# Kernel tuning notes

Measured on AMD Instinct MI355X. Metric: run time of the kernel, lower is better.

## Reference

```python
import jax, jax.numpy as jnp
import numpy as np

D, H, E, K = 1024, 1024, 8, 2  # model dim, expert hidden dim, n_experts, top_k


def setup_inputs() -> dict:
    key = jax.random.key(0)
    ks = jax.random.split(key, 5)
    s = lambda k, shape, scale: jax.random.normal(k, shape, dtype=jnp.float32) * scale
    return {
        "input_batch": s(ks[0], (2, 512, D), 1.0),
        "router_w": s(ks[1], (D, E), D ** -0.5),
        "w_in": s(ks[2], (E, D, H), D ** -0.5),
        "b_in": jnp.zeros((E, H), jnp.float32),
        "w_out": s(ks[3], (E, H, D), H ** -0.5),
        "b_out": jnp.zeros((E, D), jnp.float32),
    }


def _moe(x, router_w, w_in, b_in, w_out, b_out):
    B, S, Dm = x.shape
    T = B * S
    x2 = x.reshape(T, Dm)
    # router: per-token logit scores over experts
    logits = x2 @ router_w                                # [T, E]
    probs = jax.nn.softmax(logits, axis=-1)
    # sampler: top-k experts per token
    top_p, top_e = jax.lax.top_k(probs, K)                # [T, K]
    flat_e = top_e.reshape(-1)                            # [N] with N = T*K
    flat_p = top_p.reshape(-1)
    tok = jnp.repeat(jnp.arange(T), K)                    # owning token of each dispatch row
    # sort dispatched rows by expert id (expert_sorted_indices in the original)
    order = jnp.argsort(flat_e)
    se, sp, st = flat_e[order], flat_p[order], tok[order]
    xd = x2[st]                                           # [N, D] gathered dispatch
    N = xd.shape[0]
    # per-expert 2-layer MLP; loop over the small fixed expert set with masking
    h = jnp.zeros((N, H), x.dtype)
    for e in range(E):
        m = (se == e)[:, None]
        h = h + jnp.where(m, jax.nn.gelu(xd @ w_in[e] + b_in[e]), 0.0)
    y = jnp.zeros((N, Dm), x.dtype)
    for e in range(E):
        m = (se == e)[:, None]
        y = y + jnp.where(m, h @ w_out[e] + b_out[e], 0.0)
    # weighted scatter-combine (index_add in the original)
    y = y * sp[:, None]
    out = jnp.zeros((T, Dm), x.dtype).at[st].add(y)
    return out.reshape(B, S, Dm)


def reference(input_batch, router_w, w_in, b_in, w_out, b_out):
    return _moe(input_batch, router_w, w_in, b_in, w_out, b_out)
```

## Files before the change

### kernel.cpp

```cpp
#include <hip/hip_runtime.h>
#include <hip/hip_bf16.h>

#define DM 1024
#define HD 1024
#define NE 8
#define NT 1024
#define NR 2048
#define BM 64
#define BN 64
#define BKK 64
#define LDK 72
#define MT_MAX 40
#define PN_MAX (MT_MAX * BM)
#define NBLK (MT_MAX * (HD / BN))
#define NXCD 8

typedef __attribute__((ext_vector_type(8))) short short8;
typedef __attribute__((ext_vector_type(4))) float f32x4;

typedef const __attribute__((address_space(1))) void* gas_ptr;
typedef __attribute__((address_space(3))) void* las_ptr;

__device__ __forceinline__ void glds16(const void* g, void* l) {
    __builtin_amdgcn_global_load_lds((gas_ptr)g, (las_ptr)l, 16, 0, 0);
}

__device__ __forceinline__ float gelu_tanh(float x) {
    float x3 = x * x * x;
    return 0.5f * x * (1.0f + tanhf(0.7978845608028654f * (x + 0.044715f * x3)));
}

__global__ __launch_bounds__(256) void moe_front(const float* __restrict__ x,
                                                 const float* __restrict__ rw,
                                                 const float* __restrict__ w_in,
                                                 const float* __restrict__ w_out,
                                                 int* __restrict__ e_sel,
                                                 float* __restrict__ p_sel,
                                                 __hip_bfloat16* __restrict__ wt1,
                                                 __hip_bfloat16* __restrict__ wt2) {
    __shared__ float ts[64][65];
    int bid = blockIdx.x;
    if (bid < 4096) {
        int ty = bid >> 8;
        int bx = bid & 255;
        const float* src = (ty < 8 ? w_in : w_out) + (size_t)(ty & 7) * DM * HD;
        unsigned short* dst = (unsigned short*)(ty < 8 ? wt1 : wt2) + (size_t)(ty & 7) * DM * HD;
        int k0 = (bx >> 4) * 64, n0 = (bx & 15) * 64;
        int r = threadIdx.x >> 4;
        int c = (threadIdx.x & 15) * 4;
#pragma unroll
        for (int i = 0; i < 4; ++i) {
            int rr = r + 16 * i;
            float4 f = *(const float4*)(src + (size_t)(k0 + rr) * HD + n0 + c);
            ts[rr][c] = f.x; ts[rr][c + 1] = f.y; ts[rr][c + 2] = f.z; ts[rr][c + 3] = f.w;
        }
        __syncthreads();
#pragma unroll
        for (int i = 0; i < 4; ++i) {
            int rn = r + 16 * i;
            __hip_bfloat16 b0 = __float2bfloat16(ts[c][rn]);
            __hip_bfloat16 b1 = __float2bfloat16(ts[c + 1][rn]);
            __hip_bfloat16 b2 = __float2bfloat16(ts[c + 2][rn]);
            __hip_bfloat16 b3 = __float2bfloat16(ts[c + 3][rn]);
            ushort4 u;
            u.x = *(unsigned short*)&b0; u.y = *(unsigned short*)&b1;
            u.z = *(unsigned short*)&b2; u.w = *(unsigned short*)&b3;
            *(ushort4*)(dst + (size_t)(n0 + rn) * DM + k0 + c) = u;
        }
    } else {
        int w = threadIdx.x >> 6;
        int lane = threadIdx.x & 63;
        int t = (bid - 4096) * 4 + w;
        const float* xr = x + (size_t)t * DM;
        float acc[NE];
#pragma unroll
        for (int e = 0; e < NE; ++e) acc[e] = 0.0f;
        for (int d = lane; d < DM; d += 64) {
            float xv = xr[d];
            const float* rp = rw + (size_t)d * NE;
#pragma unroll
            for (int e = 0; e < NE; ++e) acc[e] += xv * rp[e];
        }
#pragma unroll
        for (int e = 0; e < NE; ++e) {
#pragma unroll
            for (int off = 32; off > 0; off >>= 1) acc[e] += __shfl_xor(acc[e], off);
        }
        if (lane == 0) {
            float m = acc[0];
#pragma unroll
            for (int e = 1; e < NE; ++e) m = fmaxf(m, acc[e]);
            float p[NE];
            float s = 0.0f;
#pragma unroll
            for (int e = 0; e < NE; ++e) { p[e] = __expf(acc[e] - m); s += p[e]; }
            float inv = 1.0f / s;
            int i0 = 0;
#pragma unroll
            for (int e = 1; e < NE; ++e) if (p[e] > p[i0]) i0 = e;
            int i1 = (i0 == 0) ? 1 : 0;
#pragma unroll
            for (int e = 0; e < NE; ++e) if (e != i1 && e != i0 && p[e] > p[i1]) i1 = e;
            e_sel[2 * t + 0] = i0;
            e_sel[2 * t + 1] = i1;
            p_sel[2 * t + 0] = p[i0] * inv;
            p_sel[2 * t + 1] = p[i1] * inv;
        }
    }
}

__global__ void moe_router(const float* __restrict__ x, const float* __restrict__ rw,
                           int* __restrict__ e_sel, float* __restrict__ p_sel) {
    int t = blockIdx.x;
    int lane = threadIdx.x;
    const float* xr = x + (size_t)t * DM;
    float acc[NE];
#pragma unroll
    for (int e = 0; e < NE; ++e) acc[e] = 0.0f;
    for (int d = lane; d < DM; d += 64) {
        float xv = xr[d];
        const float* r = rw + (size_t)d * NE;
#pragma unroll
        for (int e = 0; e < NE; ++e) acc[e] += xv * r[e];
    }
#pragma unroll
    for (int e = 0; e < NE; ++e) {
#pragma unroll
        for (int off = 32; off > 0; off >>= 1) acc[e] += __shfl_xor(acc[e], off);
    }
    if (lane == 0) {
        float m = acc[0];
#pragma unroll
        for (int e = 1; e < NE; ++e) m = fmaxf(m, acc[e]);
        float p[NE];
        float s = 0.0f;
#pragma unroll
        for (int e = 0; e < NE; ++e) { p[e] = __expf(acc[e] - m); s += p[e]; }
        float inv = 1.0f / s;
        int i0 = 0;
#pragma unroll
        for (int e = 1; e < NE; ++e) if (p[e] > p[i0]) i0 = e;
        int i1 = (i0 == 0) ? 1 : 0;
#pragma unroll
        for (int e = 0; e < NE; ++e) if (e != i1 && e != i0 && p[e] > p[i1]) i1 = e;
        e_sel[2 * t + 0] = i0;
        e_sel[2 * t + 1] = i1;
        p_sel[2 * t + 0] = p[i0] * inv;
        p_sel[2 * t + 1] = p[i1] * inv;
    }
}

__global__ void moe_route_pack(const int* __restrict__ e_sel, int* __restrict__ meta,
                               int* __restrict__ sorted_tok, int* __restrict__ pos_of_row) {
    __shared__ int scnt[NE];
    __shared__ int soff[NE];
    int tid = threadIdx.x;
    if (tid < NE) scnt[tid] = 0;
    __syncthreads();
    for (int i = tid; i < NR; i += 256) atomicAdd(&scnt[e_sel[i]], 1);
    __syncthreads();
    if (tid == 0) {
        int off = 0, tc = 0;
        for (int e = 0; e < NE; ++e) {
            soff[e] = off;
            meta[8 + e] = off;
            int nt = (scnt[e] + BM - 1) / BM;
            for (int t = 0; t < nt; ++t) meta[16 + tc++] = e;
            off += nt * BM;
            scnt[e] = 0;
        }
        for (; tc < MT_MAX; ++tc) meta[16 + tc] = -1;
    }
    __syncthreads();
    for (int i = tid; i < PN_MAX; i += 256) sorted_tok[i] = -1;
    __syncthreads();
    for (int i = tid; i < NR; i += 256) {
        int e = e_sel[i];
        int r = atomicAdd(&scnt[e], 1);
        int pos = soff[e] + r;
        sorted_tok[pos] = i >> 1;
        pos_of_row[i] = pos;
    }
}

__global__ __launch_bounds__(256) void moe_gather(const float* __restrict__ x,
                                                  const int* __restrict__ sorted_tok,
                                                  __hip_bfloat16* __restrict__ xg) {
    int pos = blockIdx.x;
    int t = sorted_tok[pos];
    int j = threadIdx.x * 4;
    ushort4 u;
    if (t >= 0) {
        float4 f = *(const float4*)(x + (size_t)t * DM + j);
        __hip_bfloat16 b0 = __float2bfloat16(f.x), b1 = __float2bfloat16(f.y);
        __hip_bfloat16 b2 = __float2bfloat16(f.z), b3 = __float2bfloat16(f.w);
        u.x = *(unsigned short*)&b0; u.y = *(unsigned short*)&b1;
        u.z = *(unsigned short*)&b2; u.w = *(unsigned short*)&b3;
    } else {
        u.x = u.y = u.z = u.w = 0;
    }
    *(ushort4*)((unsigned short*)xg + (size_t)pos * DM + j) = u;
}

template <int EPI>
__global__ __launch_bounds__(256, 3) void moe_gemm_async(const __hip_bfloat16* __restrict__ A,
                                                         const __hip_bfloat16* __restrict__ Bt,
                                                         const float* __restrict__ bias,
                                                         const int* __restrict__ meta,
                                                         __hip_bfloat16* __restrict__ Hout,
                                                         float* __restrict__ Yout) {
    int bid = blockIdx.x;
    int swz = (bid % NXCD) * (NBLK / NXCD) + bid / NXCD;
    int mt = swz >> 4;
    int nb = swz & 15;
    int e = meta[16 + mt];
    if (e < 0) return;

    __shared__ __align__(16) unsigned char smem[3 * 16384];

    int tid = threadIdx.x;
    int wid = tid >> 6, lane = tid & 63;
    int wm = wid >> 1, wn = wid & 1;

    const unsigned short* Ab = (const unsigned short*)A + (size_t)mt * BM * DM;
    const unsigned short* Bb = (const unsigned short*)Bt + (size_t)e * DM * HD + (size_t)nb * BN * DM;

    int srow = wid * 16 + (lane >> 3);
    int s_log = (lane & 7) ^ (lane >> 3);
    const unsigned short* agp0 = Ab + (size_t)srow * DM + s_log * 8;
    const unsigned short* agp1 = agp0 + 8 * DM;
    const unsigned short* bgp0 = Bb + (size_t)srow * DM + s_log * 8;
    const unsigned short* bgp1 = bgp0 + 8 * DM;

    auto ISSUE = [&](int b, int kt) {
        unsigned char* sa = &smem[b * 16384 + wid * 2048];
        unsigned char* sb = &smem[b * 16384 + 8192 + wid * 2048];
        glds16(agp0 + kt * BKK, sa);
        glds16(agp1 + kt * BKK, sa + 1024);
        glds16(bgp0 + kt * BKK, sb);
        glds16(bgp1 + kt * BKK, sb + 1024);
    };

    int r16 = lane & 15, g = lane >> 4, l7 = lane & 7;
    int aoff[2][2], boff[2][2];
#pragma unroll
    for (int kk = 0; kk < 2; ++kk)
#pragma unroll
        for (int f = 0; f < 2; ++f) {
            int sw = (((kk << 2) + g) ^ l7) << 4;
            aoff[kk][f] = (wm * 32 + r16 + 16 * f) * 128 + sw;
            boff[kk][f] = (wn * 32 + r16 + 16 * f) * 128 + sw;
        }

    f32x4 acc[2][2] = {};

    ISSUE(0, 0);
    ISSUE(1, 1);
    ISSUE(2, 2);

#pragma unroll
    for (int kt = 0; kt < 16; ++kt) {
        if (kt <= 13)      asm volatile("s_waitcnt vmcnt(8)" ::: "memory");
        else if (kt == 14) asm volatile("s_waitcnt vmcnt(4)" ::: "memory");
        else               asm volatile("s_waitcnt vmcnt(0)" ::: "memory");
        asm volatile("s_barrier" ::: "memory");
        const unsigned char* sa = &smem[(kt % 3) * 16384];
        const unsigned char* sb = sa + 8192;
#pragma unroll
        for (int kk = 0; kk < 2; ++kk) {
            short8 a0 = *(const short8*)(sa + aoff[kk][0]);
            short8 a1 = *(const short8*)(sa + aoff[kk][1]);
            short8 b0 = *(const short8*)(sb + boff[kk][0]);
            short8 b1 = *(const short8*)(sb + boff[kk][1]);
            acc[0][0] = __builtin_amdgcn_mfma_f32_16x16x32_bf16(a0, b0, acc[0][0], 0, 0, 0);
            acc[0][1] = __builtin_amdgcn_mfma_f32_16x16x32_bf16(a0, b1, acc[0][1], 0, 0, 0);
            acc[1][0] = __builtin_amdgcn_mfma_f32_16x16x32_bf16(a1, b0, acc[1][0], 0, 0, 0);
            acc[1][1] = __builtin_amdgcn_mfma_f32_16x16x32_bf16(a1, b1, acc[1][1], 0, 0, 0);
        }
        asm volatile("s_barrier" ::: "memory");
        if (kt + 3 < 16) ISSUE(kt % 3, kt + 3);
    }

    int row0 = mt * BM + wm * 32 + ((lane >> 4) << 2);
    int col0 = nb * BN + wn * 32 + (lane & 15);
    const float* be = bias + (size_t)e * HD;
#pragma unroll
    for (int fm = 0; fm < 2; ++fm) {
#pragma unroll
        for (int fn = 0; fn < 2; ++fn) {
            int c = col0 + fn * 16;
            float bv = be[c];
#pragma unroll
            for (int r = 0; r < 4; ++r) {
                int rr = row0 + fm * 16 + r;
                float v = acc[fm][fn][r] + bv;
                if (EPI == 0) {
                    Hout[(size_t)rr * HD + c] = __float2bfloat16(gelu_tanh(v));
                } else {
                    Yout[(size_t)rr * HD + c] = v;
                }
            }
        }
    }
}

__global__ __launch_bounds__(256) void moe_combine(const float* __restrict__ y,
                                                   const float* __restrict__ p_sel,
                                                   const int* __restrict__ pos_of_row,
                                                   float* __restrict__ out) {
    int t = blockIdx.x;
    int j = threadIdx.x * 4;
    int q0 = pos_of_row[2 * t], q1 = pos_of_row[2 * t + 1];
    float p0 = p_sel[2 * t], p1 = p_sel[2 * t + 1];
    float4 a = *(const float4*)(y + (size_t)q0 * DM + j);
    float4 b = *(const float4*)(y + (size_t)q1 * DM + j);
    float4 o;
    o.x = p0 * a.x + p1 * b.x;
    o.y = p0 * a.y + p1 * b.y;
    o.z = p0 * a.z + p1 * b.z;
    o.w = p0 * a.w + p1 * b.w;
    *(float4*)(out + (size_t)t * DM + j) = o;
}

template <int EPI>
__global__ __launch_bounds__(256) void moe_gemm(const __hip_bfloat16* __restrict__ A,
                                                const float* __restrict__ W,
                                                const float* __restrict__ bias,
                                                const int* __restrict__ meta,
                                                __hip_bfloat16* __restrict__ Hout,
                                                float* __restrict__ Yout) {
    int mt = blockIdx.y;
    int e = meta[16 + mt];
    if (e < 0) return;
    int nb = blockIdx.x;
    __shared__ __align__(16) __hip_bfloat16 As[2][BM][LDK];
    __shared__ __align__(16) __hip_bfloat16 Bs[2][BN][LDK];
    int tid = threadIdx.x;
    int wid = tid >> 6, lane = tid & 63;
    int wm = wid >> 1, wn = wid & 1;
    const __hip_bfloat16* Ab = A + (size_t)mt * BM * DM;
    const float* Wb = W + (size_t)e * DM * HD + (size_t)nb * BN;
    uint4 ra[2];
    float4 rb[4];
    auto GLOAD = [&](int kt) {
#pragma unroll
        for (int i = 0; i < 2; ++i) {
            int c = tid + 256 * i;
            int row = c >> 3, col8 = c & 7;
            ra[i] = *(const uint4*)((const unsigned short*)Ab + (size_t)row * DM + kt * BKK + col8 * 8);
        }
#pragma unroll
        for (int i = 0; i < 4; ++i) {
            int c = tid + 256 * i;
            int kr = c >> 4, c4 = c & 15;
            rb[i] = *(const float4*)(Wb + (size_t)(kt * BKK + kr) * HD + c4 * 4);
        }
    };
    auto STORE = [&](int b) {
#pragma unroll
        for (int i = 0; i < 2; ++i) {
            int c = tid + 256 * i;
            int row = c >> 3, col8 = c & 7;
            *(uint4*)&As[b][row][col8 * 8] = ra[i];
        }
#pragma unroll
        for (int i = 0; i < 4; ++i) {
            int c = tid + 256 * i;
            int kr = c >> 4, c4 = c & 15;
            Bs[b][c4 * 4 + 0][kr] = __float2bfloat16(rb[i].x);
            Bs[b][c4 * 4 + 1][kr] = __float2bfloat16(rb[i].y);
            Bs[b][c4 * 4 + 2][kr] = __float2bfloat16(rb[i].z);
            Bs[b][c4 * 4 + 3][kr] = __float2bfloat16(rb[i].w);
        }
    };
    f32x4 acc[2][2] = {};
    GLOAD(0);
    STORE(0);
    __syncthreads();
    int buf = 0;
    const int NK = DM / BKK;
    for (int kt = 0; kt < NK; ++kt) {
        if (kt + 1 < NK) GLOAD(kt + 1);
#pragma unroll
        for (int kk = 0; kk < 2; ++kk) {
            int kb = kk * 32 + (lane >> 4) * 8;
            short8 a0 = *(const short8*)&As[buf][wm * 32 + (lane & 15)][kb];
            short8 a1 = *(const short8*)&As[buf][wm * 32 + 16 + (lane & 15)][kb];
            short8 b0 = *(const short8*)&Bs[buf][wn * 32 + (lane & 15)][kb];
            short8 b1 = *(const short8*)&Bs[buf][wn * 32 + 16 + (lane & 15)][kb];
            acc[0][0] = __builtin_amdgcn_mfma_f32_16x16x32_bf16(a0, b0, acc[0][0], 0, 0, 0);
            acc[0][1] = __builtin_amdgcn_mfma_f32_16x16x32_bf16(a0, b1, acc[0][1], 0, 0, 0);
            acc[1][0] = __builtin_amdgcn_mfma_f32_16x16x32_bf16(a1, b0, acc[1][0], 0, 0, 0);
            acc[1][1] = __builtin_amdgcn_mfma_f32_16x16x32_bf16(a1, b1, acc[1][1], 0, 0, 0);
        }
        if (kt + 1 < NK) {
            STORE(buf ^ 1);
            __syncthreads();
            buf ^= 1;
        }
    }
    int row0 = mt * BM + wm * 32 + ((lane >> 4) << 2);
    int col0 = nb * BN + wn * 32 + (lane & 15);
    const float* be = bias + (size_t)e * HD;
#pragma unroll
    for (int fm = 0; fm < 2; ++fm) {
#pragma unroll
        for (int fn = 0; fn < 2; ++fn) {
            int c = col0 + fn * 16;
            float bv = be[c];
#pragma unroll
            for (int r = 0; r < 4; ++r) {
                int rr = row0 + fm * 16 + r;
                float v = acc[fm][fn][r] + bv;
                if (EPI == 0) {
                    Hout[(size_t)rr * HD + c] = __float2bfloat16(gelu_tanh(v));
                } else {
                    Yout[(size_t)rr * HD + c] = v;
                }
            }
        }
    }
}

extern "C" void kernel_launch(void* const* d_in, const int* in_sizes, int n_in,
                              void* d_out, int out_size, void* d_ws, size_t ws_size,
                              hipStream_t stream) {
    const float* x     = (const float*)d_in[0];
    const float* rw    = (const float*)d_in[1];
    const float* w_in  = (const float*)d_in[2];
    const float* b_in  = (const float*)d_in[3];
    const float* w_out = (const float*)d_in[4];
    const float* b_out = (const float*)d_in[5];
    float* out = (float*)d_out;

    char* ws = (char*)d_ws;
    int*   e_sel      = (int*)ws;
    float* p_sel      = (float*)(ws + 8 * 1024);
    int*   meta       = (int*)(ws + 16 * 1024);
    int*   sorted_tok = (int*)(ws + 17 * 1024);
    int*   pos_of_row = (int*)(ws + 27 * 1024);

    const size_t SZ_X  = (size_t)PN_MAX * DM * 2;
    const size_t SZ_Y  = (size_t)PN_MAX * DM * 4;
    const size_t SZ_WT = (size_t)NE * DM * HD * 2;

    __hip_bfloat16* xg  = (__hip_bfloat16*)(ws + 64 * 1024);
    __hip_bfloat16* h   = (__hip_bfloat16*)(ws + 64 * 1024 + SZ_X);
    __hip_bfloat16* wt1 = (__hip_bfloat16*)(ws + 64 * 1024 + 2 * SZ_X);
    float*          y   = (float*)wt1;
    __hip_bfloat16* wt2 = (__hip_bfloat16*)(ws + 64 * 1024 + 2 * SZ_X + SZ_WT);

    const size_t NEED_FULL = 64 * 1024 + 2 * SZ_X + 2 * SZ_WT;
    const size_t NEED_FB   = 64 * 1024 + 2 * SZ_X + SZ_Y;

    if (ws_size >= NEED_FULL) {
        moe_front<<<4096 + NT / 4, 256, 0, stream>>>(x, rw, w_in, w_out, e_sel, p_sel, wt1, wt2);
        moe_route_pack<<<1, 256, 0, stream>>>(e_sel, meta, sorted_tok, pos_of_row);
        moe_gather<<<PN_MAX, 256, 0, stream>>>(x, sorted_tok, xg);
        moe_gemm_async<0><<<NBLK, 256, 0, stream>>>(xg, wt1, b_in, meta, h, nullptr);
        moe_gemm_async<1><<<NBLK, 256, 0, stream>>>(h, wt2, b_out, meta, nullptr, y);
        moe_combine<<<NT, 256, 0, stream>>>(y, p_sel, pos_of_row, out);
    } else if (ws_size >= NEED_FB) {
        float* y2 = (float*)(ws + 64 * 1024 + 2 * SZ_X);
        moe_router<<<NT, 64, 0, stream>>>(x, rw, e_sel, p_sel);
        moe_route_pack<<<1, 256, 0, stream>>>(e_sel, meta, sorted_tok, pos_of_row);
        moe_gather<<<PN_MAX, 256, 0, stream>>>(x, sorted_tok, xg);
        dim3 grid(HD / BN, MT_MAX);
        moe_gemm<0><<<grid, 256, 0, stream>>>(xg, w_in, b_in, meta, h, nullptr);
        moe_gemm<1><<<grid, 256, 0, stream>>>(h, w_out, b_out, meta, nullptr, y2);
        moe_combine<<<NT, 256, 0, stream>>>(y2, p_sel, pos_of_row, out);
    }
}
```

Before: 65.62 us.

## Fuse token gather into first GEMM via indirect row loads from bf16 token copy

The bf16 conversion of the input tokens moves into the front kernel, which writes a compact token copy plus one zero padding row. The separate gather kernel launch is removed. The first expert GEMM now reads A rows indirectly through sorted_tok, and padding slots point at the zero row. This removes one kernel launch and a full write and read of the gathered activation buffer, at the cost of scattered row addresses in the GEMM's async loads.

```diff
diff --git a/kernel.cpp b/kernel.cpp
--- a/kernel.cpp
+++ b/kernel.cpp
@@ -37,7 +37,8 @@
                                                  int* __restrict__ e_sel,
                                                  float* __restrict__ p_sel,
                                                  __hip_bfloat16* __restrict__ wt1,
-                                                 __hip_bfloat16* __restrict__ wt2) {
+                                                 __hip_bfloat16* __restrict__ wt2,
+                                                 __hip_bfloat16* __restrict__ xc) {
     __shared__ float ts[64][65];
     int bid = blockIdx.x;
     if (bid < 4096) {
@@ -67,7 +68,7 @@
             u.z = *(unsigned short*)&b2; u.w = *(unsigned short*)&b3;
             *(ushort4*)(dst + (size_t)(n0 + rn) * DM + k0 + c) = u;
         }
-    } else {
+    } else if (bid < 4096 + NT / 4) {
         int w = threadIdx.x >> 6;
         int lane = threadIdx.x & 63;
         int t = (bid - 4096) * 4 + w;
@@ -106,6 +107,20 @@
             p_sel[2 * t + 0] = p[i0] * inv;
             p_sel[2 * t + 1] = p[i1] * inv;
         }
+    } else {
+        int t = bid - (4096 + NT / 4);
+        int j = threadIdx.x * 4;
+        ushort4 u;
+        if (t < NT) {
+            float4 f = *(const float4*)(x + (size_t)t * DM + j);
+            __hip_bfloat16 b0 = __float2bfloat16(f.x), b1 = __float2bfloat16(f.y);
+            __hip_bfloat16 b2 = __float2bfloat16(f.z), b3 = __float2bfloat16(f.w);
+            u.x = *(unsigned short*)&b0; u.y = *(unsigned short*)&b1;
+            u.z = *(unsigned short*)&b2; u.w = *(unsigned short*)&b3;
+        } else {
+            u.x = u.y = u.z = u.w = 0;
+        }
+        *(ushort4*)((unsigned short*)xc + (size_t)t * DM + j) = u;
     }
 }
 
@@ -172,7 +187,7 @@
         for (; tc < MT_MAX; ++tc) meta[16 + tc] = -1;
     }
     __syncthreads();
-    for (int i = tid; i < PN_MAX; i += 256) sorted_tok[i] = -1;
+    for (int i = tid; i < PN_MAX; i += 256) sorted_tok[i] = NT;
     __syncthreads();
     for (int i = tid; i < NR; i += 256) {
         int e = e_sel[i];
@@ -190,7 +205,7 @@
     int t = sorted_tok[pos];
     int j = threadIdx.x * 4;
     ushort4 u;
-    if (t >= 0) {
+    if (t >= 0 && t < NT) {
         float4 f = *(const float4*)(x + (size_t)t * DM + j);
         __hip_bfloat16 b0 = __float2bfloat16(f.x), b1 = __float2bfloat16(f.y);
         __hip_bfloat16 b2 = __float2bfloat16(f.z), b3 = __float2bfloat16(f.w);
@@ -202,11 +217,12 @@
     *(ushort4*)((unsigned short*)xg + (size_t)pos * DM + j) = u;
 }
 
-template <int EPI>
+template <int EPI, int INDIR>
 __global__ __launch_bounds__(256, 3) void moe_gemm_async(const __hip_bfloat16* __restrict__ A,
                                                          const __hip_bfloat16* __restrict__ Bt,
                                                          const float* __restrict__ bias,
                                                          const int* __restrict__ meta,
+                                                         const int* __restrict__ sorted_tok,
                                                          __hip_bfloat16* __restrict__ Hout,
                                                          float* __restrict__ Yout) {
     int bid = blockIdx.x;
@@ -222,13 +238,22 @@
     int wid = tid >> 6, lane = tid & 63;
     int wm = wid >> 1, wn = wid & 1;
 
-    const unsigned short* Ab = (const unsigned short*)A + (size_t)mt * BM * DM;
     const unsigned short* Bb = (const unsigned short*)Bt + (size_t)e * DM * HD + (size_t)nb * BN * DM;
 
     int srow = wid * 16 + (lane >> 3);
     int s_log = (lane & 7) ^ (lane >> 3);
-    const unsigned short* agp0 = Ab + (size_t)srow * DM + s_log * 8;
-    const unsigned short* agp1 = agp0 + 8 * DM;
+    const unsigned short* agp0;
+    const unsigned short* agp1;
+    if (INDIR) {
+        int tok0 = sorted_tok[mt * BM + srow];
+        int tok1 = sorted_tok[mt * BM + srow + 8];
+        agp0 = (const unsigned short*)A + (size_t)tok0 * DM + s_log * 8;
+        agp1 = (const unsigned short*)A + (size_t)tok1 * DM + s_log * 8;
+    } else {
+        const unsigned short* Ab = (const unsigned short*)A + (size_t)mt * BM * DM;
+        agp0 = Ab + (size_t)srow * DM + s_log * 8;
+        agp1 = agp0 + 8 * DM;
+    }
     const unsigned short* bgp0 = Bb + (size_t)srow * DM + s_log * 8;
     const unsigned short* bgp1 = bgp0 + 8 * DM;
 
@@ -440,34 +465,37 @@
     int*   sorted_tok = (int*)(ws + 17 * 1024);
     int*   pos_of_row = (int*)(ws + 27 * 1024);
 
+    const size_t SZ_XC = (size_t)1056 * DM * 2;
     const size_t SZ_X  = (size_t)PN_MAX * DM * 2;
     const size_t SZ_Y  = (size_t)PN_MAX * DM * 4;
     const size_t SZ_WT = (size_t)NE * DM * HD * 2;
 
-    __hip_bfloat16* xg  = (__hip_bfloat16*)(ws + 64 * 1024);
-    __hip_bfloat16* h   = (__hip_bfloat16*)(ws + 64 * 1024 + SZ_X);
-    __hip_bfloat16* wt1 = (__hip_bfloat16*)(ws + 64 * 1024 + 2 * SZ_X);
+    __hip_bfloat16* xc  = (__hip_bfloat16*)(ws + 64 * 1024);
+    __hip_bfloat16* h   = (__hip_bfloat16*)(ws + 64 * 1024 + SZ_XC);
+    __hip_bfloat16* wt1 = (__hip_bfloat16*)(ws + 64 * 1024 + SZ_XC + SZ_X);
     float*          y   = (float*)wt1;
-    __hip_bfloat16* wt2 = (__hip_bfloat16*)(ws + 64 * 1024 + 2 * SZ_X + SZ_WT);
-
-    const size_t NEED_FULL = 64 * 1024 + 2 * SZ_X + 2 * SZ_WT;
+    __hip_bfloat16* wt2 = (__hip_bfloat16*)(ws + 64 * 1024 + SZ_XC + SZ_X + SZ_WT);
+
+    const size_t NEED_FULL = 64 * 1024 + SZ_XC + SZ_X + 2 * SZ_WT;
     const size_t NEED_FB   = 64 * 1024 + 2 * SZ_X + SZ_Y;
 
     if (ws_size >= NEED_FULL) {
-        moe_front<<<4096 + NT / 4, 256, 0, stream>>>(x, rw, w_in, w_out, e_sel, p_sel, wt1, wt2);
+        moe_front<<<4096 + NT / 4 + (NT + 1), 256, 0, stream>>>(x, rw, w_in, w_out,
+                                                                e_sel, p_sel, wt1, wt2, xc);
         moe_route_pack<<<1, 256, 0, stream>>>(e_sel, meta, sorted_tok, pos_of_row);
-        moe_gather<<<PN_MAX, 256, 0, stream>>>(x, sorted_tok, xg);
-        moe_gemm_async<0><<<NBLK, 256, 0, stream>>>(xg, wt1, b_in, meta, h, nullptr);
-        moe_gemm_async<1><<<NBLK, 256, 0, stream>>>(h, wt2, b_out, meta, nullptr, y);
+        moe_gemm_async<0, 1><<<NBLK, 256, 0, stream>>>(xc, wt1, b_in, meta, sorted_tok, h, nullptr);
+        moe_gemm_async<1, 0><<<NBLK, 256, 0, stream>>>(h, wt2, b_out, meta, sorted_tok, nullptr, y);
         moe_combine<<<NT, 256, 0, stream>>>(y, p_sel, pos_of_row, out);
     } else if (ws_size >= NEED_FB) {
-        float* y2 = (float*)(ws + 64 * 1024 + 2 * SZ_X);
+        __hip_bfloat16* xg2 = (__hip_bfloat16*)(ws + 64 * 1024);
+        __hip_bfloat16* h2  = (__hip_bfloat16*)(ws + 64 * 1024 + SZ_X);
+        float* y2           = (float*)(ws + 64 * 1024 + 2 * SZ_X);
         moe_router<<<NT, 64, 0, stream>>>(x, rw, e_sel, p_sel);
         moe_route_pack<<<1, 256, 0, stream>>>(e_sel, meta, sorted_tok, pos_of_row);
-        moe_gather<<<PN_MAX, 256, 0, stream>>>(x, sorted_tok, xg);
+        moe_gather<<<PN_MAX, 256, 0, stream>>>(x, sorted_tok, xg2);
         dim3 grid(HD / BN, MT_MAX);
-        moe_gemm<0><<<grid, 256, 0, stream>>>(xg, w_in, b_in, meta, h, nullptr);
-        moe_gemm<1><<<grid, 256, 0, stream>>>(h, w_out, b_out, meta, nullptr, y2);
+        moe_gemm<0><<<grid, 256, 0, stream>>>(xg2, w_in, b_in, meta, h2, nullptr);
+        moe_gemm<1><<<grid, 256, 0, stream>>>(h2, w_out, b_out, meta, nullptr, y2);
         moe_combine<<<NT, 256, 0, stream>>>(y2, p_sel, pos_of_row, out);
     }
 }
```

After: 62.38 us (median of 2 runs). 4.9% less time.
